# Optimization experiments

Measured on AMD Instinct MI355X. Metric: run time of the kernel, lower is better.

## Reference

```python
import jax, jax.numpy as jnp
import numpy as np

B, T, D = 2, 2048, 1024
H, RANK = 16, 32
DH = D // H  # 64


def setup_inputs() -> dict:
    key = jax.random.key(0)
    ks = jax.random.split(key, 6)
    sd = 1.0 / np.sqrt(D)
    sdh = 1.0 / np.sqrt(DH)
    return {
        "x": jax.random.normal(ks[0], (B, T, D), dtype=jnp.float32),
        "W_qkv": jax.random.normal(ks[1], (D, 3 * D), dtype=jnp.float32) * sd,
        "W_q_lsr": jax.random.normal(ks[2], (H, DH, RANK), dtype=jnp.float32) * sdh,
        "W_k_lsr": jax.random.normal(ks[3], (H, DH, RANK), dtype=jnp.float32) * sdh,
        "lsr_core": jnp.ones((H, RANK), dtype=jnp.float32),
        "W_o": jax.random.normal(ks[4], (D, D), dtype=jnp.float32) * sd,
    }


def reference(x, W_qkv, W_q_lsr, W_k_lsr, lsr_core, W_o):
    b, t, d = x.shape
    # Fused QKV projection
    qkv = x @ W_qkv  # (B, T, 3D)
    q, k, v = jnp.split(qkv, 3, axis=-1)
    # (B, H, T, DH)
    q = q.reshape(b, t, H, DH).transpose(0, 2, 1, 3)
    k = k.reshape(b, t, H, DH).transpose(0, 2, 1, 3)
    v = v.reshape(b, t, H, DH).transpose(0, 2, 1, 3)
    # Low-rank bilinear score: q^T Wq diag(core) Wk^T k
    ql = jnp.einsum("bhtd,hdr->bhtr", q, W_q_lsr)  # (B, H, T, R)
    kl = jnp.einsum("bhsd,hdr->bhsr", k, W_k_lsr)  # (B, H, T, R)
    scale = 1.0 / jnp.sqrt(jnp.asarray(RANK, dtype=x.dtype))
    scores = jnp.einsum("bhtr,bhsr->bhts", ql * lsr_core[None, :, None, :], kl) * scale
    # Causal mask
    causal = jnp.tril(jnp.ones((t, t), dtype=bool))
    scores = jnp.where(causal[None, None], scores, jnp.asarray(-jnp.inf, dtype=scores.dtype))
    attn = jax.nn.softmax(scores, axis=-1)
    y = jnp.einsum("bhts,bhsd->bhtd", attn, v)  # (B, H, T, DH)
    y = y.transpose(0, 2, 1, 3).reshape(b, t, d)
    return y @ W_o
```

## Files before the change

kernel.cpp:

```cpp
#include <hip/hip_runtime.h>
#include <hip/hip_bf16.h>

#define B_  2
#define T_  2048
#define D_  1024
#define H_  16
#define DH_ 64
#define R_  32
#define BT_ (B_*T_)
#define BH_ (B_*H_)

typedef unsigned short u16;
typedef unsigned int   u32;
typedef __attribute__((ext_vector_type(8))) short bhalf8;
typedef __attribute__((ext_vector_type(4))) float floatx4;

#define WSB_FLAG  0
#define WSB_XB    256
#define WSB_WCATT (WSB_XB    + 8388608)
#define WSB_QL    (WSB_WCATT + 4194304)
#define WSB_KL    (WSB_QL    + 4194304)
#define WSB_VT    (WSB_KL    + 4194304)
#define WSB_YB    (WSB_VT    + 8388608)
#define WSB_WOT   (WSB_YB    + 8388608)

#define NEG_ -1.0e30f

__device__ __forceinline__ float bfs(u16 s) {
    union { u32 i; float f; } w; w.i = ((u32)s) << 16; return w.f;
}
__device__ __forceinline__ u16 tob(float f) {
    __hip_bfloat16 h = __float2bfloat16(f);
    return *(u16*)&h;
}
__device__ __forceinline__ u32 pack2(float a, float b) {
    return (u32)tob(a) | ((u32)tob(b) << 16);
}
__device__ __forceinline__ void gload16(const u16* g, u16* l) {
    __builtin_amdgcn_global_load_lds(
        (const __attribute__((address_space(1))) void*)g,
        (__attribute__((address_space(3))) void*)l, 16, 0, 0);
}

__global__ __launch_bounds__(64) void detect_dtype(const u32* __restrict__ xw,
                                                   int* __restrict__ flag)
{
    const int tid = threadIdx.x;
    int hits = 0;
    for (int i = tid; i < 512; i += 64) {
        const u32 w = xw[i];
        const u32 h = w & 0xFFFFu;
        const u32 e = (h >> 7) & 0xFFu;
        if (h == 0u || (e >= 100u && e <= 150u)) ++hits;
    }
    #pragma unroll
    for (int off = 32; off; off >>= 1) hits += __shfl_down(hits, off, 64);
    if (tid == 0) *flag = (hits >= 300) ? 1 : 0;
}

__global__ __launch_bounds__(256) void convert_x(
    const void* __restrict__ x, u16* __restrict__ xb,
    const int* __restrict__ flag)
{
    const int isbf = *flag;
    const int e = blockIdx.x * 256 + threadIdx.x;
    if (isbf) {
        ((uint4*)xb)[e] = ((const uint4*)x)[e];
    } else {
        float4 a0 = ((const float4*)x)[2*e];
        float4 a1 = ((const float4*)x)[2*e + 1];
        uint4 o;
        o.x = pack2(a0.x, a0.y); o.y = pack2(a0.z, a0.w);
        o.z = pack2(a1.x, a1.y); o.w = pack2(a1.z, a1.w);
        ((uint4*)xb)[e] = o;
    }
}

__global__ __launch_bounds__(256) void fold_mfma(
    const void* __restrict__ Wqkv, const void* __restrict__ Wq_lsr,
    const void* __restrict__ Wk_lsr, const void* __restrict__ core,
    u16* __restrict__ WcatT, const int* __restrict__ flag)
{
    __shared__ __align__(16) u16 Bq[128 * 72];
    __shared__ __align__(16) u16 Bk[128 * 72];
    __shared__ __align__(16) u16 Aq[32 * 72];
    __shared__ __align__(16) u16 Ak[32 * 72];
    const int isbf = *flag;
    const int tid  = threadIdx.x;
    const int lane = tid & 63;
    const int w    = tid >> 6;
    const int n16  = lane & 15;
    const int q4   = lane >> 4;
    const int h    = blockIdx.y;
    const int d0   = blockIdx.x * 128;

    #pragma unroll
    for (int p = 0; p < 8; ++p) {
        const int e  = tid + p * 256;
        const int r  = e & 31, dh = e >> 5;
        float aq, ak;
        if (isbf) {
            aq = bfs(((const u16*)Wq_lsr)[(h*DH_ + dh)*R_ + r]);
            ak = bfs(((const u16*)Wk_lsr)[(h*DH_ + dh)*R_ + r]);
        } else {
            aq = ((const float*)Wq_lsr)[(h*DH_ + dh)*R_ + r];
            ak = ((const float*)Wk_lsr)[(h*DH_ + dh)*R_ + r];
        }
        Aq[r * 72 + dh] = tob(aq);
        Ak[r * 72 + dh] = tob(ak);
    }
    #pragma unroll
    for (int p = 0; p < 8; ++p) {
        const int e  = tid + p * 256;
        const int n  = e >> 4, ch = e & 15;
        if (isbf) {
            uint2 wq = *(const uint2*)((const u16*)Wqkv + (size_t)(d0+n)*(3*D_) + h*DH_ + ch*4);
            uint2 wk = *(const uint2*)((const u16*)Wqkv + (size_t)(d0+n)*(3*D_) + D_ + h*DH_ + ch*4);
            *(uint2*)&Bq[n * 72 + ch*4] = wq;
            *(uint2*)&Bk[n * 72 + ch*4] = wk;
        } else {
            float4 fq = *(const float4*)((const float*)Wqkv + (size_t)(d0+n)*(3*D_) + h*DH_ + ch*4);
            float4 fk = *(const float4*)((const float*)Wqkv + (size_t)(d0+n)*(3*D_) + D_ + h*DH_ + ch*4);
            uint2 oq, ok;
            oq.x = pack2(fq.x, fq.y); oq.y = pack2(fq.z, fq.w);
            ok.x = pack2(fk.x, fk.y); ok.y = pack2(fk.z, fk.w);
            *(uint2*)&Bq[n * 72 + ch*4] = oq;
            *(uint2*)&Bk[n * 72 + ch*4] = ok;
        }
    }
    __syncthreads();

    floatx4 accq[2][2], acck[2][2];
    #pragma unroll
    for (int mi = 0; mi < 2; ++mi)
        #pragma unroll
        for (int ni = 0; ni < 2; ++ni) { accq[mi][ni] = (floatx4)(0.f); acck[mi][ni] = (floatx4)(0.f); }

    #pragma unroll
    for (int kk = 0; kk < 2; ++kk) {
        bhalf8 aqf[2], akf[2], bqf[2], bkf[2];
        #pragma unroll
        for (int mi = 0; mi < 2; ++mi) {
            aqf[mi] = *(const bhalf8*)&Aq[(mi*16 + n16) * 72 + kk*32 + q4*8];
            akf[mi] = *(const bhalf8*)&Ak[(mi*16 + n16) * 72 + kk*32 + q4*8];
        }
        #pragma unroll
        for (int ni = 0; ni < 2; ++ni) {
            bqf[ni] = *(const bhalf8*)&Bq[(w*32 + ni*16 + n16) * 72 + kk*32 + q4*8];
            bkf[ni] = *(const bhalf8*)&Bk[(w*32 + ni*16 + n16) * 72 + kk*32 + q4*8];
        }
        #pragma unroll
        for (int mi = 0; mi < 2; ++mi)
            #pragma unroll
            for (int ni = 0; ni < 2; ++ni) {
                accq[mi][ni] = __builtin_amdgcn_mfma_f32_16x16x32_bf16(aqf[mi], bqf[ni], accq[mi][ni], 0, 0, 0);
                acck[mi][ni] = __builtin_amdgcn_mfma_f32_16x16x32_bf16(akf[mi], bkf[ni], acck[mi][ni], 0, 0, 0);
            }
    }

    const float scale = (float)(0.17677669529663687 * 1.4426950408889634);
    #pragma unroll
    for (int mi = 0; mi < 2; ++mi) {
        #pragma unroll
        for (int rr = 0; rr < 4; ++rr) {
            const int r = mi*16 + q4*4 + rr;
            const float cc = (isbf ? bfs(((const u16*)core)[h*R_ + r])
                                   : ((const float*)core)[h*R_ + r]) * scale;
            #pragma unroll
            for (int ni = 0; ni < 2; ++ni) {
                const int d = d0 + w*32 + ni*16 + n16;
                WcatT[(size_t)(h*R_ + r) * D_ + d]       = tob(accq[mi][ni][rr] * cc);
                WcatT[(size_t)(512 + h*R_ + r) * D_ + d] = tob(acck[mi][ni][rr]);
            }
        }
    }
}

__global__ __launch_bounds__(256) void convert_T(
    const void* __restrict__ src, u16* __restrict__ dst,
    int srcStride, int srcColOff, int dstRowOff, const int* __restrict__ flag)
{
    __shared__ __align__(16) u16 tile[64 * 72];
    const int isbf = *flag;
    const int tid = threadIdx.x;
    const int j0  = blockIdx.x * 64;
    const int i0  = blockIdx.y * 64;
    #pragma unroll
    for (int p = 0; p < 2; ++p) {
        const int e = tid + p * 256;
        const int r = e >> 3, ch = e & 7;
        if (isbf) {
            uint4 w = *(const uint4*)((const u16*)src + (size_t)(i0 + r) * srcStride + srcColOff + j0 + ch*8);
            *(uint4*)&tile[r * 72 + ch*8] = w;
        } else {
            const float* s = (const float*)src + (size_t)(i0 + r) * srcStride + srcColOff + j0 + ch*8;
            float4 a0 = *(const float4*)s;
            float4 a1 = *(const float4*)(s + 4);
            uint4 o;
            o.x = pack2(a0.x, a0.y); o.y = pack2(a0.z, a0.w);
            o.z = pack2(a1.x, a1.y); o.w = pack2(a1.z, a1.w);
            *(uint4*)&tile[r * 72 + ch*8] = o;
        }
    }
    __syncthreads();
    #pragma unroll
    for (int p = 0; p < 2; ++p) {
        const int e = tid + p * 256;
        const int c = e >> 3, ch = e & 7;
        u16 tmp[8];
        #pragma unroll
        for (int j = 0; j < 8; ++j) tmp[j] = tile[(ch*8 + j) * 72 + c];
        *(uint4*)(dst + (size_t)(dstRowOff + j0 + c) * D_ + i0 + ch*8) = *(uint4*)tmp;
    }
}

__global__ __launch_bounds__(256, 2) void gemm1_mfma(
    const u16* __restrict__ xb, const u16* __restrict__ WcatT,
    u16* __restrict__ ql, u16* __restrict__ kl, u16* __restrict__ v_t)
{
    __shared__ __align__(16) u16 As[128 * 64];
    __shared__ __align__(16) u16 Bs[128 * 64];
    const int tid  = threadIdx.x;
    const int lane = tid & 63;
    const int w    = tid >> 6;
    const int n16  = lane & 15;
    const int q4   = lane >> 4;
    const int wx   = w & 1;
    const int wy   = w >> 1;
    const int bm   = blockIdx.y * 128;
    const int bn   = blockIdx.x * 128;
    const int lrow = lane >> 3;
    const int lcol = (lane & 7) * 8;

    floatx4 acc[4][4];
    #pragma unroll
    for (int i = 0; i < 4; ++i)
        #pragma unroll
        for (int j = 0; j < 4; ++j) acc[i][j] = (floatx4)(0.f);

    for (int kt = 0; kt < D_; kt += 64) {
        #pragma unroll
        for (int i = 0; i < 4; ++i) {
            const int r0 = w*32 + i*8;
            gload16(xb    + (size_t)(bm + r0 + lrow) * D_ + kt + lcol, &As[r0 * 64]);
            gload16(WcatT + (size_t)(bn + r0 + lrow) * D_ + kt + lcol, &Bs[r0 * 64]);
        }
        __syncthreads();
        #pragma unroll
        for (int kk = 0; kk < 2; ++kk) {
            bhalf8 a[4], b[4];
            #pragma unroll
            for (int mi = 0; mi < 4; ++mi)
                a[mi] = *(const bhalf8*)&As[(wy*64 + mi*16 + n16) * 64 + kk*32 + q4*8];
            #pragma unroll
            for (int ni = 0; ni < 4; ++ni)
                b[ni] = *(const bhalf8*)&Bs[(wx*64 + ni*16 + n16) * 64 + kk*32 + q4*8];
            #pragma unroll
            for (int mi = 0; mi < 4; ++mi)
                #pragma unroll
                for (int ni = 0; ni < 4; ++ni)
                    acc[mi][ni] = __builtin_amdgcn_mfma_f32_16x16x32_bf16(
                        a[mi], b[ni], acc[mi][ni], 0, 0, 0);
        }
        __syncthreads();
    }

    if (bn < 1024) {
        #pragma unroll
        for (int mi = 0; mi < 4; ++mi) {
            #pragma unroll
            for (int rr = 0; rr < 4; ++rr) {
                const int row = bm + wy*64 + mi*16 + q4*4 + rr;
                const int b   = row >> 11;
                const int t   = row & (T_ - 1);
                #pragma unroll
                for (int ni = 0; ni < 4; ++ni) {
                    const int col = bn + wx*64 + ni*16 + n16;
                    const u16 val = tob(acc[mi][ni][rr]);
                    if (col < 512) {
                        const int h = col >> 5, r = col & 31;
                        ql[((size_t)(b*H_ + h)*T_ + t)*R_ + r] = val;
                    } else {
                        const int c = col - 512; const int h = c >> 5, r = c & 31;
                        kl[((size_t)(b*H_ + h)*T_ + t)*R_ + r] = val;
                    }
                }
            }
        }
    } else {
        #pragma unroll
        for (int mi = 0; mi < 4; ++mi) {
            const int row0 = bm + wy*64 + mi*16 + q4*4;
            const int b = row0 >> 11;
            const int t = row0 & (T_ - 1);
            #pragma unroll
            for (int ni = 0; ni < 4; ++ni) {
                const int c = bn - 1024 + wx*64 + ni*16 + n16;
                const int h = c >> 6, dh = c & 63;
                uint2 o;
                o.x = pack2(acc[mi][ni][0], acc[mi][ni][1]);
                o.y = pack2(acc[mi][ni][2], acc[mi][ni][3]);
                *(uint2*)(v_t + ((size_t)(b*H_ + h) * DH_ + dh) * T_ + t) = o;
            }
        }
    }
}

__device__ __forceinline__ void softmax_update(
    floatx4 (&Sc)[8], float &mrow, float &lrow, floatx4 (&O)[4], int q4)
{
    float cmax[8];
    #pragma unroll
    for (int c = 0; c < 8; ++c)
        cmax[c] = fmaxf(fmaxf(Sc[c][0], Sc[c][1]), fmaxf(Sc[c][2], Sc[c][3]));
    float rmax = fmaxf(fmaxf(fmaxf(cmax[0], cmax[1]), fmaxf(cmax[2], cmax[3])),
                       fmaxf(fmaxf(cmax[4], cmax[5]), fmaxf(cmax[6], cmax[7])));
    rmax = fmaxf(rmax, __shfl_xor(rmax, 16, 64));
    rmax = fmaxf(rmax, __shfl_xor(rmax, 32, 64));

    const float mn = fmaxf(mrow, rmax);
    const int norescale = __all(rmax <= mrow);

    float csum[8];
    #pragma unroll
    for (int c = 0; c < 8; ++c) {
        #pragma unroll
        for (int r = 0; r < 4; ++r)
            Sc[c][r] = __builtin_amdgcn_exp2f(Sc[c][r] - mn);
        csum[c] = (Sc[c][0] + Sc[c][1]) + (Sc[c][2] + Sc[c][3]);
    }
    float rsum = ((csum[0] + csum[1]) + (csum[2] + csum[3]))
               + ((csum[4] + csum[5]) + (csum[6] + csum[7]));
    rsum += __shfl_xor(rsum, 16, 64);
    rsum += __shfl_xor(rsum, 32, 64);

    if (norescale) {
        lrow += rsum;
    } else {
        const float alpha = __builtin_amdgcn_exp2f(mrow - mn);
        mrow = mn;
        lrow = lrow * alpha + rsum;
        float aO[4];
        #pragma unroll
        for (int r = 0; r < 4; ++r) aO[r] = __shfl(alpha, q4*4 + r, 64);
        #pragma unroll
        for (int c2 = 0; c2 < 4; ++c2)
            #pragma unroll
            for (int r = 0; r < 4; ++r) O[c2][r] *= aO[r];
    }
}

__global__ __launch_bounds__(512, 4) void attn_kernel(
    const u16* __restrict__ ql, const u16* __restrict__ kl,
    const u16* __restrict__ v_t, u16* __restrict__ y)
{
    __shared__ __align__(16) u16 kls[128 * 40];
    __shared__ __align__(16) u16 vsT[64 * 136];

    const int tid  = threadIdx.x;
    const int lane = tid & 63;
    const int w    = tid >> 6;
    const int n16  = lane & 15;
    const int q4   = lane >> 4;
    const int bh   = blockIdx.x;
    const int by   = blockIdx.y;
    const int qt2  = (by < 8) ? (15 - by) : (by - 8);
    const int t0   = qt2 * 128;
    const int nt   = qt2 + 1;

    const u16* qlb = ql + (size_t)bh * T_ * R_;
    const bhalf8 aq = *(const bhalf8*)(qlb + (size_t)(t0 + w*16 + n16) * R_ + q4*8);

    const u16* klb = kl  + (size_t)bh * T_ * R_;
    const u16* vtb = v_t + (size_t)bh * DH_ * T_;
    const int rk = tid >> 2, ck = (tid & 3) * 8;
    const int dv = tid >> 4;
    const int m  = tid & 15;
    const int cv = m * 8;
    const int pb = ((m & 1) << 4) | (((m >> 1) & 1) << 2) | ((m >> 2) << 5);

    uint4 kc0 = *(const uint4*)(klb + (size_t)(rk     ) * R_ + ck);
    uint4 vc0 = *(const uint4*)(vtb + (size_t)(dv     ) * T_ + cv);
    uint4 vc1 = *(const uint4*)(vtb + (size_t)(dv + 32) * T_ + cv);
    uint4 kn0 = kc0, vn0 = vc0, vn1 = vc1;

    float mrow = NEG_, lrow = 0.f;
    floatx4 O[4];
    #pragma unroll
    for (int c = 0; c < 4; ++c) O[c] = (floatx4)(0.f);

    for (int it = 0; it < nt; ++it) {
        const int s0 = it * 128;
        __syncthreads();
        *(uint4*)&kls[rk * 40 + ck] = kc0;
        {
            uint2 t;
            t.x = vc0.x; t.y = vc0.y; *(uint2*)&vsT[(dv     ) * 136 + pb    ] = t;
            t.x = vc0.z; t.y = vc0.w; *(uint2*)&vsT[(dv     ) * 136 + pb + 8] = t;
            t.x = vc1.x; t.y = vc1.y; *(uint2*)&vsT[(dv + 32) * 136 + pb    ] = t;
            t.x = vc1.z; t.y = vc1.w; *(uint2*)&vsT[(dv + 32) * 136 + pb + 8] = t;
        }
        if (it + 1 < nt) {
            const int s1 = s0 + 128;
            kn0 = *(const uint4*)(klb + (size_t)(s1 + rk) * R_ + ck);
            vn0 = *(const uint4*)(vtb + (size_t)(dv     ) * T_ + s1 + cv);
            vn1 = *(const uint4*)(vtb + (size_t)(dv + 32) * T_ + s1 + cv);
        }
        __syncthreads();

        floatx4 Sc[8];
        #pragma unroll
        for (int c = 0; c < 8; ++c) {
            bhalf8 ak = *(const bhalf8*)&kls[(16*c + n16) * 40 + q4*8];
            Sc[c] = __builtin_amdgcn_mfma_f32_16x16x32_bf16(ak, aq, (floatx4)(0.f), 0, 0, 0);
        }

        if (it == nt - 1) {
            const int tq = w*16 + n16;
            #pragma unroll
            for (int c = 0; c < 8; ++c) {
                const int sb = 16*c + 4*q4;
                #pragma unroll
                for (int r = 0; r < 4; ++r)
                    if (sb + r > tq) Sc[c][r] = NEG_;
            }
        }

        softmax_update(Sc, mrow, lrow, O, q4);

        #pragma unroll
        for (int kc = 0; kc < 4; ++kc) {
            union { u32 wd[4]; bhalf8 v; } pu;
            pu.wd[0] = pack2(Sc[2*kc    ][0], Sc[2*kc    ][1]);
            pu.wd[1] = pack2(Sc[2*kc    ][2], Sc[2*kc    ][3]);
            pu.wd[2] = pack2(Sc[2*kc + 1][0], Sc[2*kc + 1][1]);
            pu.wd[3] = pack2(Sc[2*kc + 1][2], Sc[2*kc + 1][3]);
            const bhalf8 pa = pu.v;
            #pragma unroll
            for (int c2 = 0; c2 < 4; ++c2) {
                bhalf8 bv = *(const bhalf8*)&vsT[(16*c2 + n16) * 136 + kc*32 + q4*8];
                O[c2] = __builtin_amdgcn_mfma_f32_16x16x32_bf16(pa, bv, O[c2], 0, 0, 0);
            }
        }

        kc0 = kn0; vc0 = vn0; vc1 = vn1;
    }

    const int b = bh >> 4, h = bh & 15;
    float lb[4];
    #pragma unroll
    for (int r = 0; r < 4; ++r) lb[r] = __shfl(lrow, q4*4 + r, 64);
    #pragma unroll
    for (int r = 0; r < 4; ++r) {
        const float rl = 1.0f / lb[r];
        const int t = t0 + w*16 + q4*4 + r;
        #pragma unroll
        for (int c2 = 0; c2 < 4; ++c2)
            y[((size_t)b * T_ + t) * D_ + h * DH_ + 16*c2 + n16] = tob(O[c2][r] * rl);
    }
}

__global__ __launch_bounds__(256, 2) void out_gemm_mfma(
    const u16* __restrict__ yb, const u16* __restrict__ WoT,
    float* __restrict__ out)
{
    __shared__ __align__(16) u16 As[128 * 64];
    __shared__ __align__(16) u16 Bs[64 * 64];
    const int tid  = threadIdx.x;
    const int lane = tid & 63;
    const int w    = tid >> 6;
    const int n16  = lane & 15;
    const int q4   = lane >> 4;
    const int wx   = w & 1;
    const int wy   = w >> 1;
    const int bm   = blockIdx.y * 128;
    const int bn   = blockIdx.x * 64;
    const int lrow = lane >> 3;
    const int lcol = (lane & 7) * 8;

    floatx4 acc[4][2];
    #pragma unroll
    for (int i = 0; i < 4; ++i)
        #pragma unroll
        for (int j = 0; j < 2; ++j) acc[i][j] = (floatx4)(0.f);

    for (int kt = 0; kt < D_; kt += 64) {
        #pragma unroll
        for (int i = 0; i < 4; ++i) {
            const int r0 = w*32 + i*8;
            gload16(yb + (size_t)(bm + r0 + lrow) * D_ + kt + lcol, &As[r0 * 64]);
        }
        #pragma unroll
        for (int i = 0; i < 2; ++i) {
            const int r0 = w*16 + i*8;
            gload16(WoT + (size_t)(bn + r0 + lrow) * D_ + kt + lcol, &Bs[r0 * 64]);
        }
        __syncthreads();
        #pragma unroll
        for (int kk = 0; kk < 2; ++kk) {
            bhalf8 a[4], b[2];
            #pragma unroll
            for (int mi = 0; mi < 4; ++mi)
                a[mi] = *(const bhalf8*)&As[(wy*64 + mi*16 + n16) * 64 + kk*32 + q4*8];
            #pragma unroll
            for (int ni = 0; ni < 2; ++ni)
                b[ni] = *(const bhalf8*)&Bs[(wx*32 + ni*16 + n16) * 64 + kk*32 + q4*8];
            #pragma unroll
            for (int mi = 0; mi < 4; ++mi)
                #pragma unroll
                for (int ni = 0; ni < 2; ++ni)
                    acc[mi][ni] = __builtin_amdgcn_mfma_f32_16x16x32_bf16(
                        a[mi], b[ni], acc[mi][ni], 0, 0, 0);
        }
        __syncthreads();
    }

    #pragma unroll
    for (int mi = 0; mi < 4; ++mi) {
        #pragma unroll
        for (int rr = 0; rr < 4; ++rr) {
            const int row = bm + wy*64 + mi*16 + q4*4 + rr;
            #pragma unroll
            for (int ni = 0; ni < 2; ++ni) {
                const int col = bn + wx*32 + ni*16 + n16;
                out[(size_t)row * D_ + col] = acc[mi][ni][rr];
            }
        }
    }
}

extern "C" void kernel_launch(void* const* d_in, const int* in_sizes, int n_in,
                              void* d_out, int out_size, void* d_ws, size_t ws_size,
                              hipStream_t stream)
{
    (void)out_size; (void)ws_size;
    const void* in_x = nullptr; const void* in_wqkv = nullptr;
    const void* in_wq = nullptr; const void* in_wk = nullptr;
    const void* in_core = nullptr; const void* in_wo = nullptr;
    for (int i = 0; i < n_in; ++i) {
        const int s = in_sizes[i];
        if      (s == BT_*D_)     { if (!in_x)    in_x    = d_in[i]; }
        else if (s == D_*3*D_)    { if (!in_wqkv) in_wqkv = d_in[i]; }
        else if (s == H_*DH_*R_)  { if (!in_wq)   in_wq   = d_in[i]; else if (!in_wk) in_wk = d_in[i]; }
        else if (s == H_*R_)      { if (!in_core) in_core = d_in[i]; }
        else if (s == D_*D_)      { if (!in_wo)   in_wo   = d_in[i]; }
    }
    if (!in_x)    in_x    = d_in[0];
    if (!in_wqkv) in_wqkv = d_in[1];
    if (!in_wq)   in_wq   = d_in[2];
    if (!in_wk)   in_wk   = d_in[3];
    if (!in_core) in_core = d_in[4];
    if (!in_wo)   in_wo   = d_in[5];

    float* out = (float*)d_out;

    char* ws    = (char*)d_ws;
    int*  flag  = (int*)(ws + WSB_FLAG);
    u16*  xb    = (u16*)(ws + WSB_XB);
    u16*  WcatT = (u16*)(ws + WSB_WCATT);
    u16*  ql    = (u16*)(ws + WSB_QL);
    u16*  kl    = (u16*)(ws + WSB_KL);
    u16*  v_t   = (u16*)(ws + WSB_VT);
    u16*  yb    = (u16*)(ws + WSB_YB);
    u16*  WoT   = (u16*)(ws + WSB_WOT);

    detect_dtype<<<1, 64, 0, stream>>>((const u32*)in_x, flag);
    convert_x<<<2048, 256, 0, stream>>>(in_x, xb, flag);
    fold_mfma<<<dim3(8, 16), 256, 0, stream>>>(in_wqkv, in_wq, in_wk, in_core, WcatT, flag);
    convert_T<<<dim3(16,16), 256, 0, stream>>>(in_wqkv, WcatT, 3*D_, 2*D_, 1024, flag);
    convert_T<<<dim3(16,16), 256, 0, stream>>>(in_wo,   WoT,   D_,   0,    0,    flag);
    gemm1_mfma<<<dim3(16, 32), 256, 0, stream>>>(xb, WcatT, ql, kl, v_t);
    attn_kernel<<<dim3(32, 16), 512, 0, stream>>>(ql, kl, v_t, yb);
    out_gemm_mfma<<<dim3(16, 32), 256, 0, stream>>>(yb, WoT, out);
}
```

Baseline: 185.0 us.

## Fuse prep kernels, inline dtype detection, and shrink GEMM tiles for occupancy

The standalone dtype-detection kernel goes away, and every kernel now recomputes the bf16 flag with a warp reduction. The x conversion and the two weight transposes are merged into one launch. The QKV GEMM tile narrows from 128x128 to 128x64 and the output GEMM tile drops to 64x64, with launch bounds raised to 4 blocks per CU, so both grids get larger. The goal is fewer launches and better CU fill, at the cost of less data reuse per tile and some repeated detection work in each block.

Result: no change. 183.0 us (-1.1%).

```diff
diff --git a/kernel.cpp b/kernel.cpp
--- a/kernel.cpp
+++ b/kernel.cpp
@@ -41,53 +41,93 @@
         (const __attribute__((address_space(1))) void*)g,
         (__attribute__((address_space(3))) void*)l, 16, 0, 0);
 }
-
-__global__ __launch_bounds__(64) void detect_dtype(const u32* __restrict__ xw,
-                                                   int* __restrict__ flag)
-{
-    const int tid = threadIdx.x;
+__device__ __forceinline__ int detect_isbf(const u32* __restrict__ xw, int lane) {
     int hits = 0;
-    for (int i = tid; i < 512; i += 64) {
-        const u32 w = xw[i];
+    #pragma unroll
+    for (int i = 0; i < 8; ++i) {
+        const u32 w = xw[lane + i * 64];
         const u32 h = w & 0xFFFFu;
         const u32 e = (h >> 7) & 0xFFu;
         if (h == 0u || (e >= 100u && e <= 150u)) ++hits;
     }
     #pragma unroll
     for (int off = 32; off; off >>= 1) hits += __shfl_down(hits, off, 64);
-    if (tid == 0) *flag = (hits >= 300) ? 1 : 0;
-}
-
-__global__ __launch_bounds__(256) void convert_x(
+    return __shfl(hits, 0, 64) >= 300;
+}
+
+__global__ __launch_bounds__(256) void convert_fused(
     const void* __restrict__ x, u16* __restrict__ xb,
-    const int* __restrict__ flag)
-{
-    const int isbf = *flag;
-    const int e = blockIdx.x * 256 + threadIdx.x;
-    if (isbf) {
-        ((uint4*)xb)[e] = ((const uint4*)x)[e];
-    } else {
-        float4 a0 = ((const float4*)x)[2*e];
-        float4 a1 = ((const float4*)x)[2*e + 1];
-        uint4 o;
-        o.x = pack2(a0.x, a0.y); o.y = pack2(a0.z, a0.w);
-        o.z = pack2(a1.x, a1.y); o.w = pack2(a1.z, a1.w);
-        ((uint4*)xb)[e] = o;
+    const void* __restrict__ Wqkv, const void* __restrict__ Wo,
+    u16* __restrict__ WcatT, u16* __restrict__ WoT)
+{
+    __shared__ __align__(16) u16 tile[64 * 72];
+    const int tid  = threadIdx.x;
+    const int lane = tid & 63;
+    const int isbf = detect_isbf((const u32*)x, lane);
+    const int blk  = blockIdx.x;
+
+    if (blk < 2048) {
+        const int e = blk * 256 + tid;
+        if (isbf) {
+            ((uint4*)xb)[e] = ((const uint4*)x)[e];
+        } else {
+            float4 a0 = ((const float4*)x)[2*e];
+            float4 a1 = ((const float4*)x)[2*e + 1];
+            uint4 o;
+            o.x = pack2(a0.x, a0.y); o.y = pack2(a0.z, a0.w);
+            o.z = pack2(a1.x, a1.y); o.w = pack2(a1.z, a1.w);
+            ((uint4*)xb)[e] = o;
+        }
+        return;
+    }
+
+    int t = blk - 2048;
+    const void* src; u16* dst; int srcStride, srcColOff, dstRowOff;
+    if (t < 256) { src = Wqkv; dst = WcatT; srcStride = 3*D_; srcColOff = 2*D_; dstRowOff = 1024; }
+    else { t -= 256; src = Wo; dst = WoT; srcStride = D_; srcColOff = 0; dstRowOff = 0; }
+    const int j0 = (t & 15) * 64;
+    const int i0 = (t >> 4) * 64;
+    #pragma unroll
+    for (int p = 0; p < 2; ++p) {
+        const int e = tid + p * 256;
+        const int r = e >> 3, ch = e & 7;
+        if (isbf) {
+            uint4 w = *(const uint4*)((const u16*)src + (size_t)(i0 + r) * srcStride + srcColOff + j0 + ch*8);
+            *(uint4*)&tile[r * 72 + ch*8] = w;
+        } else {
+            const float* s = (const float*)src + (size_t)(i0 + r) * srcStride + srcColOff + j0 + ch*8;
+            float4 a0 = *(const float4*)s;
+            float4 a1 = *(const float4*)(s + 4);
+            uint4 o;
+            o.x = pack2(a0.x, a0.y); o.y = pack2(a0.z, a0.w);
+            o.z = pack2(a1.x, a1.y); o.w = pack2(a1.z, a1.w);
+            *(uint4*)&tile[r * 72 + ch*8] = o;
+        }
+    }
+    __syncthreads();
+    #pragma unroll
+    for (int p = 0; p < 2; ++p) {
+        const int e = tid + p * 256;
+        const int c = e >> 3, ch = e & 7;
+        u16 tmp[8];
+        #pragma unroll
+        for (int j = 0; j < 8; ++j) tmp[j] = tile[(ch*8 + j) * 72 + c];
+        *(uint4*)(dst + (size_t)(dstRowOff + j0 + c) * D_ + i0 + ch*8) = *(uint4*)tmp;
     }
 }
 
 __global__ __launch_bounds__(256) void fold_mfma(
     const void* __restrict__ Wqkv, const void* __restrict__ Wq_lsr,
     const void* __restrict__ Wk_lsr, const void* __restrict__ core,
-    u16* __restrict__ WcatT, const int* __restrict__ flag)
+    u16* __restrict__ WcatT, const void* __restrict__ x)
 {
     __shared__ __align__(16) u16 Bq[128 * 72];
     __shared__ __align__(16) u16 Bk[128 * 72];
     __shared__ __align__(16) u16 Aq[32 * 72];
     __shared__ __align__(16) u16 Ak[32 * 72];
-    const int isbf = *flag;
     const int tid  = threadIdx.x;
     const int lane = tid & 63;
+    const int isbf = detect_isbf((const u32*)x, lane);
     const int w    = tid >> 6;
     const int n16  = lane & 15;
     const int q4   = lane >> 4;
@@ -176,293 +216,9 @@
     }
 }
 
-__global__ __launch_bounds__(256) void convert_T(
-    const void* __restrict__ src, u16* __restrict__ dst,
-    int srcStride, int srcColOff, int dstRowOff, const int* __restrict__ flag)
-{
-    __shared__ __align__(16) u16 tile[64 * 72];
-    const int isbf = *flag;
-    const int tid = threadIdx.x;
-    const int j0  = blockIdx.x * 64;
-    const int i0  = blockIdx.y * 64;
-    #pragma unroll
-    for (int p = 0; p < 2; ++p) {
-        const int e = tid + p * 256;
-        const int r = e >> 3, ch = e & 7;
-        if (isbf) {
-            uint4 w = *(const uint4*)((const u16*)src + (size_t)(i0 + r) * srcStride + srcColOff + j0 + ch*8);
-            *(uint4*)&tile[r * 72 + ch*8] = w;
-        } else {
-            const float* s = (const float*)src + (size_t)(i0 + r) * srcStride + srcColOff + j0 + ch*8;
-            float4 a0 = *(const float4*)s;
-            float4 a1 = *(const float4*)(s + 4);
-            uint4 o;
-            o.x = pack2(a0.x, a0.y); o.y = pack2(a0.z, a0.w);
-            o.z = pack2(a1.x, a1.y); o.w = pack2(a1.z, a1.w);
-            *(uint4*)&tile[r * 72 + ch*8] = o;
-        }
-    }
-    __syncthreads();
-    #pragma unroll
-    for (int p = 0; p < 2; ++p) {
-        const int e = tid + p * 256;
-        const int c = e >> 3, ch = e & 7;
-        u16 tmp[8];
-        #pragma unroll
-        for (int j = 0; j < 8; ++j) tmp[j] = tile[(ch*8 + j) * 72 + c];
-        *(uint4*)(dst + (size_t)(dstRowOff + j0 + c) * D_ + i0 + ch*8) = *(uint4*)tmp;
-    }
-}
-
-__global__ __launch_bounds__(256, 2) void gemm1_mfma(
+__global__ __launch_bounds__(256, 4) void gemm1_mfma(
     const u16* __restrict__ xb, const u16* __restrict__ WcatT,
     u16* __restrict__ ql, u16* __restrict__ kl, u16* __restrict__ v_t)
-{
-    __shared__ __align__(16) u16 As[128 * 64];
-    __shared__ __align__(16) u16 Bs[128 * 64];
-    const int tid  = threadIdx.x;
-    const int lane = tid & 63;
-    const int w    = tid >> 6;
-    const int n16  = lane & 15;
-    const int q4   = lane >> 4;
-    const int wx   = w & 1;
-    const int wy   = w >> 1;
-    const int bm   = blockIdx.y * 128;
-    const int bn   = blockIdx.x * 128;
-    const int lrow = lane >> 3;
-    const int lcol = (lane & 7) * 8;
-
-    floatx4 acc[4][4];
-    #pragma unroll
-    for (int i = 0; i < 4; ++i)
-        #pragma unroll
-        for (int j = 0; j < 4; ++j) acc[i][j] = (floatx4)(0.f);
-
-    for (int kt = 0; kt < D_; kt += 64) {
-        #pragma unroll
-        for (int i = 0; i < 4; ++i) {
-            const int r0 = w*32 + i*8;
-            gload16(xb    + (size_t)(bm + r0 + lrow) * D_ + kt + lcol, &As[r0 * 64]);
-            gload16(WcatT + (size_t)(bn + r0 + lrow) * D_ + kt + lcol, &Bs[r0 * 64]);
-        }
-        __syncthreads();
-        #pragma unroll
-        for (int kk = 0; kk < 2; ++kk) {
-            bhalf8 a[4], b[4];
-            #pragma unroll
-            for (int mi = 0; mi < 4; ++mi)
-                a[mi] = *(const bhalf8*)&As[(wy*64 + mi*16 + n16) * 64 + kk*32 + q4*8];
-            #pragma unroll
-            for (int ni = 0; ni < 4; ++ni)
-                b[ni] = *(const bhalf8*)&Bs[(wx*64 + ni*16 + n16) * 64 + kk*32 + q4*8];
-            #pragma unroll
-            for (int mi = 0; mi < 4; ++mi)
-                #pragma unroll
-                for (int ni = 0; ni < 4; ++ni)
-                    acc[mi][ni] = __builtin_amdgcn_mfma_f32_16x16x32_bf16(
-                        a[mi], b[ni], acc[mi][ni], 0, 0, 0);
-        }
-        __syncthreads();
-    }
-
-    if (bn < 1024) {
-        #pragma unroll
-        for (int mi = 0; mi < 4; ++mi) {
-            #pragma unroll
-            for (int rr = 0; rr < 4; ++rr) {
-                const int row = bm + wy*64 + mi*16 + q4*4 + rr;
-                const int b   = row >> 11;
-                const int t   = row & (T_ - 1);
-                #pragma unroll
-                for (int ni = 0; ni < 4; ++ni) {
-                    const int col = bn + wx*64 + ni*16 + n16;
-                    const u16 val = tob(acc[mi][ni][rr]);
-                    if (col < 512) {
-                        const int h = col >> 5, r = col & 31;
-                        ql[((size_t)(b*H_ + h)*T_ + t)*R_ + r] = val;
-                    } else {
-                        const int c = col - 512; const int h = c >> 5, r = c & 31;
-                        kl[((size_t)(b*H_ + h)*T_ + t)*R_ + r] = val;
-                    }
-                }
-            }
-        }
-    } else {
-        #pragma unroll
-        for (int mi = 0; mi < 4; ++mi) {
-            const int row0 = bm + wy*64 + mi*16 + q4*4;
-            const int b = row0 >> 11;
-            const int t = row0 & (T_ - 1);
-            #pragma unroll
-            for (int ni = 0; ni < 4; ++ni) {
-                const int c = bn - 1024 + wx*64 + ni*16 + n16;
-                const int h = c >> 6, dh = c & 63;
-                uint2 o;
-                o.x = pack2(acc[mi][ni][0], acc[mi][ni][1]);
-                o.y = pack2(acc[mi][ni][2], acc[mi][ni][3]);
-                *(uint2*)(v_t + ((size_t)(b*H_ + h) * DH_ + dh) * T_ + t) = o;
-            }
-        }
-    }
-}
-
-__device__ __forceinline__ void softmax_update(
-    floatx4 (&Sc)[8], float &mrow, float &lrow, floatx4 (&O)[4], int q4)
-{
-    float cmax[8];
-    #pragma unroll
-    for (int c = 0; c < 8; ++c)
-        cmax[c] = fmaxf(fmaxf(Sc[c][0], Sc[c][1]), fmaxf(Sc[c][2], Sc[c][3]));
-    float rmax = fmaxf(fmaxf(fmaxf(cmax[0], cmax[1]), fmaxf(cmax[2], cmax[3])),
-                       fmaxf(fmaxf(cmax[4], cmax[5]), fmaxf(cmax[6], cmax[7])));
-    rmax = fmaxf(rmax, __shfl_xor(rmax, 16, 64));
-    rmax = fmaxf(rmax, __shfl_xor(rmax, 32, 64));
-
-    const float mn = fmaxf(mrow, rmax);
-    const int norescale = __all(rmax <= mrow);
-
-    float csum[8];
-    #pragma unroll
-    for (int c = 0; c < 8; ++c) {
-        #pragma unroll
-        for (int r = 0; r < 4; ++r)
-            Sc[c][r] = __builtin_amdgcn_exp2f(Sc[c][r] - mn);
-        csum[c] = (Sc[c][0] + Sc[c][1]) + (Sc[c][2] + Sc[c][3]);
-    }
-    float rsum = ((csum[0] + csum[1]) + (csum[2] + csum[3]))
-               + ((csum[4] + csum[5]) + (csum[6] + csum[7]));
-    rsum += __shfl_xor(rsum, 16, 64);
-    rsum += __shfl_xor(rsum, 32, 64);
-
-    if (norescale) {
-        lrow += rsum;
-    } else {
-        const float alpha = __builtin_amdgcn_exp2f(mrow - mn);
-        mrow = mn;
-        lrow = lrow * alpha + rsum;
-        float aO[4];
-        #pragma unroll
-        for (int r = 0; r < 4; ++r) aO[r] = __shfl(alpha, q4*4 + r, 64);
-        #pragma unroll
-        for (int c2 = 0; c2 < 4; ++c2)
-            #pragma unroll
-            for (int r = 0; r < 4; ++r) O[c2][r] *= aO[r];
-    }
-}
-
-__global__ __launch_bounds__(512, 4) void attn_kernel(
-    const u16* __restrict__ ql, const u16* __restrict__ kl,
-    const u16* __restrict__ v_t, u16* __restrict__ y)
-{
-    __shared__ __align__(16) u16 kls[128 * 40];
-    __shared__ __align__(16) u16 vsT[64 * 136];
-
-    const int tid  = threadIdx.x;
-    const int lane = tid & 63;
-    const int w    = tid >> 6;
-    const int n16  = lane & 15;
-    const int q4   = lane >> 4;
-    const int bh   = blockIdx.x;
-    const int by   = blockIdx.y;
-    const int qt2  = (by < 8) ? (15 - by) : (by - 8);
-    const int t0   = qt2 * 128;
-    const int nt   = qt2 + 1;
-
-    const u16* qlb = ql + (size_t)bh * T_ * R_;
-    const bhalf8 aq = *(const bhalf8*)(qlb + (size_t)(t0 + w*16 + n16) * R_ + q4*8);
-
-    const u16* klb = kl  + (size_t)bh * T_ * R_;
-    const u16* vtb = v_t + (size_t)bh * DH_ * T_;
-    const int rk = tid >> 2, ck = (tid & 3) * 8;
-    const int dv = tid >> 4;
-    const int m  = tid & 15;
-    const int cv = m * 8;
-    const int pb = ((m & 1) << 4) | (((m >> 1) & 1) << 2) | ((m >> 2) << 5);
-
-    uint4 kc0 = *(const uint4*)(klb + (size_t)(rk     ) * R_ + ck);
-    uint4 vc0 = *(const uint4*)(vtb + (size_t)(dv     ) * T_ + cv);
-    uint4 vc1 = *(const uint4*)(vtb + (size_t)(dv + 32) * T_ + cv);
-    uint4 kn0 = kc0, vn0 = vc0, vn1 = vc1;
-
-    float mrow = NEG_, lrow = 0.f;
-    floatx4 O[4];
-    #pragma unroll
-    for (int c = 0; c < 4; ++c) O[c] = (floatx4)(0.f);
-
-    for (int it = 0; it < nt; ++it) {
-        const int s0 = it * 128;
-        __syncthreads();
-        *(uint4*)&kls[rk * 40 + ck] = kc0;
-        {
-            uint2 t;
-            t.x = vc0.x; t.y = vc0.y; *(uint2*)&vsT[(dv     ) * 136 + pb    ] = t;
-            t.x = vc0.z; t.y = vc0.w; *(uint2*)&vsT[(dv     ) * 136 + pb + 8] = t;
-            t.x = vc1.x; t.y = vc1.y; *(uint2*)&vsT[(dv + 32) * 136 + pb    ] = t;
-            t.x = vc1.z; t.y = vc1.w; *(uint2*)&vsT[(dv + 32) * 136 + pb + 8] = t;
-        }
-        if (it + 1 < nt) {
-            const int s1 = s0 + 128;
-            kn0 = *(const uint4*)(klb + (size_t)(s1 + rk) * R_ + ck);
-            vn0 = *(const uint4*)(vtb + (size_t)(dv     ) * T_ + s1 + cv);
-            vn1 = *(const uint4*)(vtb + (size_t)(dv + 32) * T_ + s1 + cv);
-        }
-        __syncthreads();
-
-        floatx4 Sc[8];
-        #pragma unroll
-        for (int c = 0; c < 8; ++c) {
-            bhalf8 ak = *(const bhalf8*)&kls[(16*c + n16) * 40 + q4*8];
-            Sc[c] = __builtin_amdgcn_mfma_f32_16x16x32_bf16(ak, aq, (floatx4)(0.f), 0, 0, 0);
-        }
-
-        if (it == nt - 1) {
-            const int tq = w*16 + n16;
-            #pragma unroll
-            for (int c = 0; c < 8; ++c) {
-                const int sb = 16*c + 4*q4;
-                #pragma unroll
-                for (int r = 0; r < 4; ++r)
-                    if (sb + r > tq) Sc[c][r] = NEG_;
-            }
-        }
-
-        softmax_update(Sc, mrow, lrow, O, q4);
-
-        #pragma unroll
-        for (int kc = 0; kc < 4; ++kc) {
-            union { u32 wd[4]; bhalf8 v; } pu;
-            pu.wd[0] = pack2(Sc[2*kc    ][0], Sc[2*kc    ][1]);
-            pu.wd[1] = pack2(Sc[2*kc    ][2], Sc[2*kc    ][3]);
-            pu.wd[2] = pack2(Sc[2*kc + 1][0], Sc[2*kc + 1][1]);
-            pu.wd[3] = pack2(Sc[2*kc + 1][2], Sc[2*kc + 1][3]);
-            const bhalf8 pa = pu.v;
-            #pragma unroll
-            for (int c2 = 0; c2 < 4; ++c2) {
-                bhalf8 bv = *(const bhalf8*)&vsT[(16*c2 + n16) * 136 + kc*32 + q4*8];
-                O[c2] = __builtin_amdgcn_mfma_f32_16x16x32_bf16(pa, bv, O[c2], 0, 0, 0);
-            }
-        }
-
-        kc0 = kn0; vc0 = vn0; vc1 = vn1;
-    }
-
-    const int b = bh >> 4, h = bh & 15;
-    float lb[4];
-    #pragma unroll
-    for (int r = 0; r < 4; ++r) lb[r] = __shfl(lrow, q4*4 + r, 64);
-    #pragma unroll
-    for (int r = 0; r < 4; ++r) {
-        const float rl = 1.0f / lb[r];
-        const int t = t0 + w*16 + q4*4 + r;
-        #pragma unroll
-        for (int c2 = 0; c2 < 4; ++c2)
-            y[((size_t)b * T_ + t) * D_ + h * DH_ + 16*c2 + n16] = tob(O[c2][r] * rl);
-    }
-}
-
-__global__ __launch_bounds__(256, 2) void out_gemm_mfma(
-    const u16* __restrict__ yb, const u16* __restrict__ WoT,
-    float* __restrict__ out)
 {
     __shared__ __align__(16) u16 As[128 * 64];
     __shared__ __align__(16) u16 Bs[64 * 64];
@@ -488,12 +244,12 @@
         #pragma unroll
         for (int i = 0; i < 4; ++i) {
             const int r0 = w*32 + i*8;
-            gload16(yb + (size_t)(bm + r0 + lrow) * D_ + kt + lcol, &As[r0 * 64]);
+            gload16(xb + (size_t)(bm + r0 + lrow) * D_ + kt + lcol, &As[r0 * 64]);
         }
         #pragma unroll
         for (int i = 0; i < 2; ++i) {
             const int r0 = w*16 + i*8;
-            gload16(WoT + (size_t)(bn + r0 + lrow) * D_ + kt + lcol, &Bs[r0 * 64]);
+            gload16(WcatT + (size_t)(bn + r0 + lrow) * D_ + kt + lcol, &Bs[r0 * 64]);
         }
         __syncthreads();
         #pragma unroll
@@ -515,11 +271,257 @@
         __syncthreads();
     }
 
-    #pragma unroll
-    for (int mi = 0; mi < 4; ++mi) {
+    if (bn < 1024) {
+        #pragma unroll
+        for (int mi = 0; mi < 4; ++mi) {
+            #pragma unroll
+            for (int rr = 0; rr < 4; ++rr) {
+                const int row = bm + wy*64 + mi*16 + q4*4 + rr;
+                const int b   = row >> 11;
+                const int t   = row & (T_ - 1);
+                #pragma unroll
+                for (int ni = 0; ni < 2; ++ni) {
+                    const int col = bn + wx*32 + ni*16 + n16;
+                    const u16 val = tob(acc[mi][ni][rr]);
+                    if (col < 512) {
+                        const int h = col >> 5, r = col & 31;
+                        ql[((size_t)(b*H_ + h)*T_ + t)*R_ + r] = val;
+                    } else {
+                        const int c = col - 512; const int h = c >> 5, r = c & 31;
+                        kl[((size_t)(b*H_ + h)*T_ + t)*R_ + r] = val;
+                    }
+                }
+            }
+        }
+    } else {
+        #pragma unroll
+        for (int mi = 0; mi < 4; ++mi) {
+            const int row0 = bm + wy*64 + mi*16 + q4*4;
+            const int b = row0 >> 11;
+            const int t = row0 & (T_ - 1);
+            #pragma unroll
+            for (int ni = 0; ni < 2; ++ni) {
+                const int c = bn - 1024 + wx*32 + ni*16 + n16;
+                const int h = c >> 6, dh = c & 63;
+                uint2 o;
+                o.x = pack2(acc[mi][ni][0], acc[mi][ni][1]);
+                o.y = pack2(acc[mi][ni][2], acc[mi][ni][3]);
+                *(uint2*)(v_t + ((size_t)(b*H_ + h) * DH_ + dh) * T_ + t) = o;
+            }
+        }
+    }
+}
+
+__device__ __forceinline__ void softmax_update(
+    floatx4 (&Sc)[8], float &mrow, float &lrow, floatx4 (&O)[4], int q4)
+{
+    float cmax[8];
+    #pragma unroll
+    for (int c = 0; c < 8; ++c)
+        cmax[c] = fmaxf(fmaxf(Sc[c][0], Sc[c][1]), fmaxf(Sc[c][2], Sc[c][3]));
+    float rmax = fmaxf(fmaxf(fmaxf(cmax[0], cmax[1]), fmaxf(cmax[2], cmax[3])),
+                       fmaxf(fmaxf(cmax[4], cmax[5]), fmaxf(cmax[6], cmax[7])));
+    rmax = fmaxf(rmax, __shfl_xor(rmax, 16, 64));
+    rmax = fmaxf(rmax, __shfl_xor(rmax, 32, 64));
+
+    const float mn = fmaxf(mrow, rmax);
+    const int norescale = __all(rmax <= mrow);
+
+    float csum[8];
+    #pragma unroll
+    for (int c = 0; c < 8; ++c) {
+        #pragma unroll
+        for (int r = 0; r < 4; ++r)
+            Sc[c][r] = __builtin_amdgcn_exp2f(Sc[c][r] - mn);
+        csum[c] = (Sc[c][0] + Sc[c][1]) + (Sc[c][2] + Sc[c][3]);
+    }
+    float rsum = ((csum[0] + csum[1]) + (csum[2] + csum[3]))
+               + ((csum[4] + csum[5]) + (csum[6] + csum[7]));
+    rsum += __shfl_xor(rsum, 16, 64);
+    rsum += __shfl_xor(rsum, 32, 64);
+
+    if (norescale) {
+        lrow += rsum;
+    } else {
+        const float alpha = __builtin_amdgcn_exp2f(mrow - mn);
+        mrow = mn;
+        lrow = lrow * alpha + rsum;
+        float aO[4];
+        #pragma unroll
+        for (int r = 0; r < 4; ++r) aO[r] = __shfl(alpha, q4*4 + r, 64);
+        #pragma unroll
+        for (int c2 = 0; c2 < 4; ++c2)
+            #pragma unroll
+            for (int r = 0; r < 4; ++r) O[c2][r] *= aO[r];
+    }
+}
+
+__global__ __launch_bounds__(512, 4) void attn_kernel(
+    const u16* __restrict__ ql, const u16* __restrict__ kl,
+    const u16* __restrict__ v_t, u16* __restrict__ y)
+{
+    __shared__ __align__(16) u16 kls[128 * 40];
+    __shared__ __align__(16) u16 vsT[64 * 136];
+
+    const int tid  = threadIdx.x;
+    const int lane = tid & 63;
+    const int w    = tid >> 6;
+    const int n16  = lane & 15;
+    const int q4   = lane >> 4;
+    const int bh   = blockIdx.x;
+    const int by   = blockIdx.y;
+    const int qt2  = (by < 8) ? (15 - by) : (by - 8);
+    const int t0   = qt2 * 128;
+    const int nt   = qt2 + 1;
+
+    const u16* qlb = ql + (size_t)bh * T_ * R_;
+    const bhalf8 aq = *(const bhalf8*)(qlb + (size_t)(t0 + w*16 + n16) * R_ + q4*8);
+
+    const u16* klb = kl  + (size_t)bh * T_ * R_;
+    const u16* vtb = v_t + (size_t)bh * DH_ * T_;
+    const int rk = tid >> 2, ck = (tid & 3) * 8;
+    const int dv = tid >> 4;
+    const int m  = tid & 15;
+    const int cv = m * 8;
+    const int pb = ((m & 1) << 4) | (((m >> 1) & 1) << 2) | ((m >> 2) << 5);
+
+    uint4 kc0 = *(const uint4*)(klb + (size_t)(rk     ) * R_ + ck);
+    uint4 vc0 = *(const uint4*)(vtb + (size_t)(dv     ) * T_ + cv);
+    uint4 vc1 = *(const uint4*)(vtb + (size_t)(dv + 32) * T_ + cv);
+    uint4 kn0 = kc0, vn0 = vc0, vn1 = vc1;
+
+    float mrow = NEG_, lrow = 0.f;
+    floatx4 O[4];
+    #pragma unroll
+    for (int c = 0; c < 4; ++c) O[c] = (floatx4)(0.f);
+
+    for (int it = 0; it < nt; ++it) {
+        const int s0 = it * 128;
+        __syncthreads();
+        *(uint4*)&kls[rk * 40 + ck] = kc0;
+        {
+            uint2 t;
+            t.x = vc0.x; t.y = vc0.y; *(uint2*)&vsT[(dv     ) * 136 + pb    ] = t;
+            t.x = vc0.z; t.y = vc0.w; *(uint2*)&vsT[(dv     ) * 136 + pb + 8] = t;
+            t.x = vc1.x; t.y = vc1.y; *(uint2*)&vsT[(dv + 32) * 136 + pb    ] = t;
+            t.x = vc1.z; t.y = vc1.w; *(uint2*)&vsT[(dv + 32) * 136 + pb + 8] = t;
+        }
+        if (it + 1 < nt) {
+            const int s1 = s0 + 128;
+            kn0 = *(const uint4*)(klb + (size_t)(s1 + rk) * R_ + ck);
+            vn0 = *(const uint4*)(vtb + (size_t)(dv     ) * T_ + s1 + cv);
+            vn1 = *(const uint4*)(vtb + (size_t)(dv + 32) * T_ + s1 + cv);
+        }
+        __syncthreads();
+
+        floatx4 Sc[8];
+        #pragma unroll
+        for (int c = 0; c < 8; ++c) {
+            bhalf8 ak = *(const bhalf8*)&kls[(16*c + n16) * 40 + q4*8];
+            Sc[c] = __builtin_amdgcn_mfma_f32_16x16x32_bf16(ak, aq, (floatx4)(0.f), 0, 0, 0);
+        }
+
+        if (it == nt - 1) {
+            const int tq = w*16 + n16;
+            #pragma unroll
+            for (int c = 0; c < 8; ++c) {
+                const int sb = 16*c + 4*q4;
+                #pragma unroll
+                for (int r = 0; r < 4; ++r)
+                    if (sb + r > tq) Sc[c][r] = NEG_;
+            }
+        }
+
+        softmax_update(Sc, mrow, lrow, O, q4);
+
+        #pragma unroll
+        for (int kc = 0; kc < 4; ++kc) {
+            union { u32 wd[4]; bhalf8 v; } pu;
+            pu.wd[0] = pack2(Sc[2*kc    ][0], Sc[2*kc    ][1]);
+            pu.wd[1] = pack2(Sc[2*kc    ][2], Sc[2*kc    ][3]);
+            pu.wd[2] = pack2(Sc[2*kc + 1][0], Sc[2*kc + 1][1]);
+            pu.wd[3] = pack2(Sc[2*kc + 1][2], Sc[2*kc + 1][3]);
+            const bhalf8 pa = pu.v;
+            #pragma unroll
+            for (int c2 = 0; c2 < 4; ++c2) {
+                bhalf8 bv = *(const bhalf8*)&vsT[(16*c2 + n16) * 136 + kc*32 + q4*8];
+                O[c2] = __builtin_amdgcn_mfma_f32_16x16x32_bf16(pa, bv, O[c2], 0, 0, 0);
+            }
+        }
+
+        kc0 = kn0; vc0 = vn0; vc1 = vn1;
+    }
+
+    const int b = bh >> 4, h = bh & 15;
+    float lb[4];
+    #pragma unroll
+    for (int r = 0; r < 4; ++r) lb[r] = __shfl(lrow, q4*4 + r, 64);
+    #pragma unroll
+    for (int r = 0; r < 4; ++r) {
+        const float rl = 1.0f / lb[r];
+        const int t = t0 + w*16 + q4*4 + r;
+        #pragma unroll
+        for (int c2 = 0; c2 < 4; ++c2)
+            y[((size_t)b * T_ + t) * D_ + h * DH_ + 16*c2 + n16] = tob(O[c2][r] * rl);
+    }
+}
+
+__global__ __launch_bounds__(256, 4) void out_gemm_mfma(
+    const u16* __restrict__ yb, const u16* __restrict__ WoT,
+    float* __restrict__ out)
+{
+    __shared__ __align__(16) u16 As[64 * 64];
+    __shared__ __align__(16) u16 Bs[64 * 64];
+    const int tid  = threadIdx.x;
+    const int lane = tid & 63;
+    const int w    = tid >> 6;
+    const int n16  = lane & 15;
+    const int q4   = lane >> 4;
+    const int wx   = w & 1;
+    const int wy   = w >> 1;
+    const int bm   = blockIdx.y * 64;
+    const int bn   = blockIdx.x * 64;
+    const int lrow = lane >> 3;
+    const int lcol = (lane & 7) * 8;
+
+    floatx4 acc[2][2];
+    #pragma unroll
+    for (int i = 0; i < 2; ++i)
+        #pragma unroll
+        for (int j = 0; j < 2; ++j) acc[i][j] = (floatx4)(0.f);
+
+    for (int kt = 0; kt < D_; kt += 64) {
+        #pragma unroll
+        for (int i = 0; i < 2; ++i) {
+            const int r0 = w*16 + i*8;
+            gload16(yb  + (size_t)(bm + r0 + lrow) * D_ + kt + lcol, &As[r0 * 64]);
+            gload16(WoT + (size_t)(bn + r0 + lrow) * D_ + kt + lcol, &Bs[r0 * 64]);
+        }
+        __syncthreads();
+        #pragma unroll
+        for (int kk = 0; kk < 2; ++kk) {
+            bhalf8 a[2], b[2];
+            #pragma unroll
+            for (int mi = 0; mi < 2; ++mi)
+                a[mi] = *(const bhalf8*)&As[(wy*32 + mi*16 + n16) * 64 + kk*32 + q4*8];
+            #pragma unroll
+            for (int ni = 0; ni < 2; ++ni)
+                b[ni] = *(const bhalf8*)&Bs[(wx*32 + ni*16 + n16) * 64 + kk*32 + q4*8];
+            #pragma unroll
+            for (int mi = 0; mi < 2; ++mi)
+                #pragma unroll
+                for (int ni = 0; ni < 2; ++ni)
+                    acc[mi][ni] = __builtin_amdgcn_mfma_f32_16x16x32_bf16(
+                        a[mi], b[ni], acc[mi][ni], 0, 0, 0);
+        }
+        __syncthreads();
+    }
+
+    #pragma unroll
+    for (int mi = 0; mi < 2; ++mi) {
         #pragma unroll
         for (int rr = 0; rr < 4; ++rr) {
-            const int row = bm + wy*64 + mi*16 + q4*4 + rr;
+            const int row = bm + wy*32 + mi*16 + q4*4 + rr;
             #pragma unroll
             for (int ni = 0; ni < 2; ++ni) {
                 const int col = bn + wx*32 + ni*16 + n16;
@@ -555,7 +557,6 @@
     float* out = (float*)d_out;
 
     char* ws    = (char*)d_ws;
-    int*  flag  = (int*)(ws + WSB_FLAG);
     u16*  xb    = (u16*)(ws + WSB_XB);
     u16*  WcatT = (u16*)(ws + WSB_WCATT);
     u16*  ql    = (u16*)(ws + WSB_QL);
@@ -564,12 +565,9 @@
     u16*  yb    = (u16*)(ws + WSB_YB);
     u16*  WoT   = (u16*)(ws + WSB_WOT);
 
-    detect_dtype<<<1, 64, 0, stream>>>((const u32*)in_x, flag);
-    convert_x<<<2048, 256, 0, stream>>>(in_x, xb, flag);
-    fold_mfma<<<dim3(8, 16), 256, 0, stream>>>(in_wqkv, in_wq, in_wk, in_core, WcatT, flag);
-    convert_T<<<dim3(16,16), 256, 0, stream>>>(in_wqkv, WcatT, 3*D_, 2*D_, 1024, flag);
-    convert_T<<<dim3(16,16), 256, 0, stream>>>(in_wo,   WoT,   D_,   0,    0,    flag);
-    gemm1_mfma<<<dim3(16, 32), 256, 0, stream>>>(xb, WcatT, ql, kl, v_t);
+    convert_fused<<<2560, 256, 0, stream>>>(in_x, xb, in_wqkv, in_wo, WcatT, WoT);
+    fold_mfma<<<dim3(8, 16), 256, 0, stream>>>(in_wqkv, in_wq, in_wk, in_core, WcatT, in_x);
+    gemm1_mfma<<<dim3(32, 32), 256, 0, stream>>>(xb, WcatT, ql, kl, v_t);
     attn_kernel<<<dim3(32, 16), 512, 0, stream>>>(ql, kl, v_t, yb);
-    out_gemm_mfma<<<dim3(16, 32), 256, 0, stream>>>(yb, WoT, out);
-}
+    out_gemm_mfma<<<dim3(16, 64), 256, 0, stream>>>(yb, WoT, out);
+}
```
